# Performance work log

Measured on AMD Instinct MI355X. Metric: run time of the kernel, lower is better.

## Reference

```python
import jax, jax.numpy as jnp
import numpy as np

N_NODES = 40000
N_EDGES = 1_600_000
F_DIM = 64          # num_features per node; MLP input is 2*F_DIM = 128
HIDDEN = 64
BETA = 1.0          # temperature tmp passed to concrete_sample


def setup_inputs() -> dict:
    key = jax.random.key(0)
    k_e, k_n, k_w1, k_w2 = jax.random.split(key, 4)
    # unique edge list (matches torch COO->dense semantics exactly: no duplicate coords)
    rng = np.random.default_rng(0)
    keys = np.unique(rng.integers(0, N_NODES * N_NODES, size=int(N_EDGES * 1.1), dtype=np.int64))
    assert keys.size >= N_EDGES
    keys = keys[:N_EDGES]
    col = jnp.asarray((keys // N_NODES).astype(np.int32))
    row = jnp.asarray((keys % N_NODES).astype(np.int32))
    embed = jax.random.normal(k_e, (N_NODES, F_DIM), jnp.float32)
    # torch.rand noise for the concrete/gumbel-sigmoid sample (kept strictly inside (0,1))
    noise = jax.random.uniform(k_n, (N_EDGES,), jnp.float32, 1e-6, 1.0 - 1e-6)
    lim1 = 1.0 / np.sqrt(2 * F_DIM)
    W1 = jax.random.uniform(k_w1, (2 * F_DIM, HIDDEN), jnp.float32, -lim1, lim1)
    b1 = jnp.zeros((HIDDEN,), jnp.float32)
    lim2 = 1.0 / np.sqrt(HIDDEN)
    W2 = jax.random.uniform(k_w2, (HIDDEN, 1), jnp.float32, -lim2, lim2)
    b2 = jnp.zeros((1,), jnp.float32)
    return {"embed": embed, "W1": W1, "b1": b1, "W2": W2, "b2": b2,
            "noise": noise, "col": col, "row": row}


def reference(embed, W1, b1, W2, b2, noise, col, row):
    # --- gather + concat + 2-layer MLP (elayers) ---
    f12 = jnp.concatenate([embed[col], embed[row]], axis=-1)   # [E, 2F]
    h = jax.nn.relu(f12 @ W1 + b1)                              # [E, 64]
    log_alpha = (h @ W2 + b2).reshape(-1)                       # [E]
    # --- concrete_sample, training=True, sample_bias=0 ---
    gate = jnp.log(noise) - jnp.log1p(-noise)
    values = jax.nn.sigmoid((gate + log_alpha) / BETA)          # sparse_mask_values
    # --- symmetrization: sym = (M + M^T)/2 gathered back at (col,row) ---
    # Equivalent to torch's sparse->dense->transpose->gather, but done sparsely
    # via a reverse-edge lookup on sorted pair keys (edges are unique).
    n = embed.shape[0]
    keys = col * n + row                                        # int32-safe: n*n < 2^31
    order = jnp.argsort(keys)
    skeys = keys[order]
    svals = values[order]
    rkeys = row * n + col
    pos = jnp.clip(jnp.searchsorted(skeys, rkeys), 0, keys.shape[0] - 1)
    rev = jnp.where(skeys[pos] == rkeys, svals[pos], jnp.float32(0.0))
    edge_mask = (values + rev) * 0.5
    return edge_mask
```

## Files before the change

kernel.cpp:

```cpp
#include <hip/hip_runtime.h>
#include <hip/hip_bf16.h>


typedef __attribute__((ext_vector_type(2))) float f32x2;

#define EPAD 68

__global__ __launch_bounds__(256) void precompute_kernel(
        const float* __restrict__ embed,
        const float* __restrict__ W1,
        const float* __restrict__ b1,
        unsigned* __restrict__ Ptop,
        unsigned* __restrict__ Pbot,
        const int* __restrict__ col,
        int* __restrict__ rowptr,
        int n_nodes, int n_edges, int gemm_blocks) {
    int t = threadIdx.x;

    if ((int)blockIdx.x >= gemm_blocks) {
        int v = (blockIdx.x - gemm_blocks) * 256 + t;
        if (v <= n_nodes) {
            int lo = 0, hi = n_edges;
            while (lo < hi) {
                int mid = (lo + hi) >> 1;
                if (col[mid] < v) lo = mid + 1; else hi = mid;
            }
            rowptr[v] = lo;
        }
        return;
    }

    __shared__ float W1s[128 * 64];
    __shared__ float E[64 * EPAD];
    int base = blockIdx.x * 64;

#pragma unroll
    for (int i = 0; i < 8; ++i) {
        int idx = i * 256 + t;
        ((float4*)W1s)[idx] = ((const float4*)W1)[idx];
    }
#pragma unroll
    for (int i = 0; i < 4; ++i) {
        int fi = i * 256 + t;
        int n = fi >> 4;
        int k4 = (fi & 15) * 4;
        float4 v;
        if (base + n < n_nodes)
            v = ((const float4*)(embed + (size_t)(base + n) * 64))[fi & 15];
        else
            v = make_float4(0.f, 0.f, 0.f, 0.f);
        *((float4*)(E + n * EPAD + k4)) = v;
    }
    __syncthreads();

    int tj = t & 15, tn = t >> 4;
    int j4 = tj * 4, n4 = tn * 4;
    float4 b1v = *(const float4*)(b1 + j4);
    float4 at[4], ab[4];
#pragma unroll
    for (int i = 0; i < 4; ++i) {
        at[i] = b1v;
        ab[i] = make_float4(0.f, 0.f, 0.f, 0.f);
    }

#pragma unroll 2
    for (int k4 = 0; k4 < 64; k4 += 4) {
        float4 e[4], wt[4], wb[4];
#pragma unroll
        for (int i = 0; i < 4; ++i) {
            e[i]  = *(const float4*)(E + (n4 + i) * EPAD + k4);
            wt[i] = *(const float4*)(W1s + (k4 + i) * 64 + j4);
            wb[i] = *(const float4*)(W1s + (64 + k4 + i) * 64 + j4);
        }
#pragma unroll
        for (int n = 0; n < 4; ++n) {
#pragma unroll
            for (int kk = 0; kk < 4; ++kk) {
                float ev = (kk == 0) ? e[n].x : (kk == 1) ? e[n].y
                         : (kk == 2) ? e[n].z : e[n].w;
                at[n].x += ev * wt[kk].x;  at[n].y += ev * wt[kk].y;
                at[n].z += ev * wt[kk].z;  at[n].w += ev * wt[kk].w;
                ab[n].x += ev * wb[kk].x;  ab[n].y += ev * wb[kk].y;
                ab[n].z += ev * wb[kk].z;  ab[n].w += ev * wb[kk].w;
            }
        }
    }

#pragma unroll
    for (int i = 0; i < 4; ++i) {
        int node = base + n4 + i;
        if (node >= n_nodes) break;
        int wt8 = __builtin_amdgcn_cvt_pk_fp8_f32(at[i].x, at[i].y, 0, false);
        wt8     = __builtin_amdgcn_cvt_pk_fp8_f32(at[i].z, at[i].w, wt8, true);
        Ptop[(size_t)node * 16 + tj] = (unsigned)wt8;
        int wb8 = __builtin_amdgcn_cvt_pk_fp8_f32(ab[i].x, ab[i].y, 0, false);
        wb8     = __builtin_amdgcn_cvt_pk_fp8_f32(ab[i].z, ab[i].w, wb8, true);
        Pbot[(size_t)node * 16 + tj] = (unsigned)wb8;
    }
}

#define DOTW(au, bu, wp, acc0, acc1) do {                             \
    f32x2 alo = __builtin_amdgcn_cvt_pk_f32_fp8((au), false);         \
    f32x2 ahi = __builtin_amdgcn_cvt_pk_f32_fp8((au), true);          \
    f32x2 blo = __builtin_amdgcn_cvt_pk_f32_fp8((bu), false);         \
    f32x2 bhi = __builtin_amdgcn_cvt_pk_f32_fp8((bu), true);          \
    f32x2 s0 = alo + blo, s1 = ahi + bhi;                             \
    s0 = __builtin_elementwise_max(s0, (f32x2)0.f);                   \
    s1 = __builtin_elementwise_max(s1, (f32x2)0.f);                   \
    acc0 += s0 * ((const f32x2*)(wp))[0];                             \
    acc1 += s1 * ((const f32x2*)(wp))[1];                             \
} while (0)

__global__ void edge_value_kernel(const uint4* __restrict__ Ptop,
                                  const uint4* __restrict__ Pbot,
                                  const float* __restrict__ W2,
                                  const float* __restrict__ b2,
                                  const float* __restrict__ noise,
                                  const int* __restrict__ col,
                                  const int* __restrict__ row,
                                  unsigned short* __restrict__ row16,
                                  unsigned short* __restrict__ vals16,
                                  int n_edges) {
    int e = blockIdx.x * blockDim.x + threadIdx.x;
    if (e >= n_edges) return;
    int c = col[e], r = row[e];
    const uint4* pt = Ptop + (size_t)c * 4;
    const uint4* pb = Pbot + (size_t)r * 4;
    f32x2 acc0 = {b2[0], 0.f}, acc1 = {0.f, 0.f};
    f32x2 acc2 = {0.f, 0.f},  acc3 = {0.f, 0.f};
#pragma unroll
    for (int g = 0; g < 4; ++g) {
        uint4 a = pt[g];
        uint4 b = pb[g];
        const float* w = W2 + g * 16;
        DOTW(a.x, b.x, w,      acc0, acc1);
        DOTW(a.y, b.y, w + 4,  acc2, acc3);
        DOTW(a.z, b.z, w + 8,  acc0, acc1);
        DOTW(a.w, b.w, w + 12, acc2, acc3);
    }
    f32x2 acc = (acc0 + acc1) + (acc2 + acc3);
    float la = acc.x + acc.y;
    float u = noise[e];
    float v = u / (u + (1.f - u) * __expf(-la));
    unsigned q = (unsigned)(v * 65535.f + 0.5f);
    if (q > 65535u) q = 65535u;
    row16[e]  = (unsigned short)r;
    vals16[e] = (unsigned short)q;
}

__device__ __forceinline__ float rev_scan(const unsigned short* __restrict__ row16,
                                          const unsigned short* __restrict__ vals16,
                                          int c, int lo, int hi, int g, int rv) {
    if (rv < c) {
        while (++g < hi) { rv = row16[g]; if (rv >= c) break; }
        return (g < hi && rv == c) ? (float)vals16[g] : 0.f;
    } else {
        while (rv > c && g > lo) rv = row16[--g];
        return (rv == c) ? (float)vals16[g] : 0.f;
    }
}

__global__ __launch_bounds__(256) void symmetrize_kernel(
        const int* __restrict__ col,
        const unsigned short* __restrict__ row16,
        const unsigned short* __restrict__ vals16,
        const int* __restrict__ rowptr,
        float* __restrict__ out,
        int n_edges, float inv_n) {
    int t = threadIdx.x;
    int e0 = blockIdx.x * 1024 + t;
    int c[4], r[4], lo[4], hi[4], g[4], pr[4];
    float vq[4];
    bool p[4], s[4];

#pragma unroll
    for (int i = 0; i < 4; ++i) {
        int e = e0 + i * 256;
        p[i] = e < n_edges;
        c[i] = 0; r[i] = 0; vq[i] = 0.f;
        if (p[i]) {
            c[i]  = col[e];
            r[i]  = row16[e];
            vq[i] = (float)vals16[e];
        }
    }
#pragma unroll
    for (int i = 0; i < 4; ++i) {
        lo[i] = 0; hi[i] = 0;
        if (p[i]) { lo[i] = rowptr[r[i]]; hi[i] = rowptr[r[i] + 1]; }
    }
#pragma unroll
    for (int i = 0; i < 4; ++i) {
        s[i] = p[i] && hi[i] > lo[i];
        g[i] = 0; pr[i] = 0;
        if (s[i]) {
            g[i] = lo[i] + (int)((float)c[i] * (float)(hi[i] - lo[i]) * inv_n);
            if (g[i] >= hi[i]) g[i] = hi[i] - 1;
            pr[i] = row16[g[i]];
        }
    }
#pragma unroll
    for (int i = 0; i < 4; ++i) {
        if (!p[i]) continue;
        float rev = s[i] ? rev_scan(row16, vals16, c[i], lo[i], hi[i], g[i], pr[i]) : 0.f;
        out[e0 + i * 256] = (vq[i] + rev) * (0.5f / 65535.f);
    }
}

extern "C" void kernel_launch(void* const* d_in, const int* in_sizes, int n_in,
                              void* d_out, int out_size, void* d_ws, size_t ws_size,
                              hipStream_t stream) {
    const float* embed = (const float*)d_in[0];
    const float* W1    = (const float*)d_in[1];
    const float* b1    = (const float*)d_in[2];
    const float* W2    = (const float*)d_in[3];
    const float* b2    = (const float*)d_in[4];
    const float* noise = (const float*)d_in[5];
    const int*   col   = (const int*)d_in[6];
    const int*   row   = (const int*)d_in[7];

    int n_nodes = in_sizes[0] / 64;
    int n_edges = in_sizes[5];
    float* out = (float*)d_out;

    char* ws = (char*)d_ws;
    size_t p_sz   = (size_t)n_nodes * 16 * sizeof(unsigned);
    size_t e16_sz = (size_t)n_edges * sizeof(unsigned short);
    unsigned*       Ptop   = (unsigned*)ws;
    unsigned*       Pbot   = (unsigned*)(ws + p_sz);
    unsigned short* row16  = (unsigned short*)(ws + 2 * p_sz);
    unsigned short* vals16 = (unsigned short*)(ws + 2 * p_sz + e16_sz);
    int*            rowptr = (int*)(ws + 2 * p_sz + 2 * e16_sz);

    int gemm_blocks = (n_nodes + 63) / 64;
    int rp_blocks   = (n_nodes + 256) / 256;

    precompute_kernel<<<gemm_blocks + rp_blocks, 256, 0, stream>>>(
        embed, W1, b1, Ptop, Pbot, col, rowptr, n_nodes, n_edges, gemm_blocks);

    edge_value_kernel<<<(n_edges + 255) / 256, 256, 0, stream>>>(
        (const uint4*)Ptop, (const uint4*)Pbot, W2, b2, noise, col, row,
        row16, vals16, n_edges);

    symmetrize_kernel<<<(n_edges + 1023) / 1024, 256, 0, stream>>>(
        col, row16, vals16, rowptr, out, n_edges, 1.0f / (float)n_nodes);
}
```

Before: 71.75 us.

## Fuse edge MLP and symmetrization, recomputing reverse-edge value instead of storing

Merges the edge-value and symmetrize kernels into one launch. Each thread finds its reverse edge and recomputes that edge's MLP and sigmoid from the per-node fp8 projections and noise, rather than reading a quantized vals16 array. The row16 conversion moves into extra blocks of the precompute kernel. This removes one launch, the vals16 round-trip and the 16-bit value quantization, at the cost of doing the MLP a second time for reverse edges and adding random gathers of Ptop/Pbot and noise.

```diff
diff --git a/kernel.cpp b/kernel.cpp
--- a/kernel.cpp
+++ b/kernel.cpp
@@ -13,12 +13,32 @@
         unsigned* __restrict__ Ptop,
         unsigned* __restrict__ Pbot,
         const int* __restrict__ col,
+        const int* __restrict__ row,
         int* __restrict__ rowptr,
-        int n_nodes, int n_edges, int gemm_blocks) {
+        unsigned short* __restrict__ row16,
+        int n_nodes, int n_edges, int gemm_blocks, int rp_blocks) {
     int t = threadIdx.x;
-
-    if ((int)blockIdx.x >= gemm_blocks) {
-        int v = (blockIdx.x - gemm_blocks) * 256 + t;
+    int bid = blockIdx.x;
+
+    if (bid >= gemm_blocks + rp_blocks) {
+        int gt = (bid - gemm_blocks - rp_blocks) * 256 + t;
+        int e8 = gt * 8;
+        if (e8 + 7 < n_edges) {
+            int4 r0 = ((const int4*)(row + e8))[0];
+            int4 r1 = ((const int4*)(row + e8))[1];
+            uint4 packed;
+            packed.x = (unsigned)r0.x | ((unsigned)r0.y << 16);
+            packed.y = (unsigned)r0.z | ((unsigned)r0.w << 16);
+            packed.z = (unsigned)r1.x | ((unsigned)r1.y << 16);
+            packed.w = (unsigned)r1.z | ((unsigned)r1.w << 16);
+            *(uint4*)(row16 + e8) = packed;
+        } else {
+            for (int e = e8; e < n_edges; ++e) row16[e] = (unsigned short)row[e];
+        }
+        return;
+    }
+    if (bid >= gemm_blocks) {
+        int v = (bid - gemm_blocks) * 256 + t;
         if (v <= n_nodes) {
             int lo = 0, hi = n_edges;
             while (lo < hi) {
@@ -32,7 +52,7 @@
 
     __shared__ float W1s[128 * 64];
     __shared__ float E[64 * EPAD];
-    int base = blockIdx.x * 64;
+    int base = bid * 64;
 
 #pragma unroll
     for (int i = 0; i < 8; ++i) {
@@ -111,23 +131,12 @@
     acc1 += s1 * ((const f32x2*)(wp))[1];                             \
 } while (0)
 
-__global__ void edge_value_kernel(const uint4* __restrict__ Ptop,
-                                  const uint4* __restrict__ Pbot,
-                                  const float* __restrict__ W2,
-                                  const float* __restrict__ b2,
-                                  const float* __restrict__ noise,
-                                  const int* __restrict__ col,
-                                  const int* __restrict__ row,
-                                  unsigned short* __restrict__ row16,
-                                  unsigned short* __restrict__ vals16,
-                                  int n_edges) {
-    int e = blockIdx.x * blockDim.x + threadIdx.x;
-    if (e >= n_edges) return;
-    int c = col[e], r = row[e];
-    const uint4* pt = Ptop + (size_t)c * 4;
-    const uint4* pb = Pbot + (size_t)r * 4;
-    f32x2 acc0 = {b2[0], 0.f}, acc1 = {0.f, 0.f};
-    f32x2 acc2 = {0.f, 0.f},  acc3 = {0.f, 0.f};
+__device__ __forceinline__ float mlp_sigmoid(const uint4* __restrict__ pt,
+                                             const uint4* __restrict__ pb,
+                                             const float* __restrict__ W2,
+                                             float b2v, float u) {
+    f32x2 acc0 = {b2v, 0.f}, acc1 = {0.f, 0.f};
+    f32x2 acc2 = {0.f, 0.f}, acc3 = {0.f, 0.f};
 #pragma unroll
     for (int g = 0; g < 4; ++g) {
         uint4 a = pt[g];
@@ -140,71 +149,55 @@
     }
     f32x2 acc = (acc0 + acc1) + (acc2 + acc3);
     float la = acc.x + acc.y;
-    float u = noise[e];
-    float v = u / (u + (1.f - u) * __expf(-la));
-    unsigned q = (unsigned)(v * 65535.f + 0.5f);
-    if (q > 65535u) q = 65535u;
-    row16[e]  = (unsigned short)r;
-    vals16[e] = (unsigned short)q;
-}
-
-__device__ __forceinline__ float rev_scan(const unsigned short* __restrict__ row16,
-                                          const unsigned short* __restrict__ vals16,
-                                          int c, int lo, int hi, int g, int rv) {
-    if (rv < c) {
-        while (++g < hi) { rv = row16[g]; if (rv >= c) break; }
-        return (g < hi && rv == c) ? (float)vals16[g] : 0.f;
-    } else {
-        while (rv > c && g > lo) rv = row16[--g];
-        return (rv == c) ? (float)vals16[g] : 0.f;
-    }
-}
-
-__global__ __launch_bounds__(256) void symmetrize_kernel(
+    return u / (u + (1.f - u) * __expf(-la));
+}
+
+__global__ __launch_bounds__(256) void fused_edge_kernel(
+        const uint4* __restrict__ Ptop,
+        const uint4* __restrict__ Pbot,
+        const float* __restrict__ W2,
+        const float* __restrict__ b2,
+        const float* __restrict__ noise,
         const int* __restrict__ col,
+        const int* __restrict__ row,
         const unsigned short* __restrict__ row16,
-        const unsigned short* __restrict__ vals16,
         const int* __restrict__ rowptr,
         float* __restrict__ out,
         int n_edges, float inv_n) {
-    int t = threadIdx.x;
-    int e0 = blockIdx.x * 1024 + t;
-    int c[4], r[4], lo[4], hi[4], g[4], pr[4];
-    float vq[4];
-    bool p[4], s[4];
-
-#pragma unroll
-    for (int i = 0; i < 4; ++i) {
-        int e = e0 + i * 256;
-        p[i] = e < n_edges;
-        c[i] = 0; r[i] = 0; vq[i] = 0.f;
-        if (p[i]) {
-            c[i]  = col[e];
-            r[i]  = row16[e];
-            vq[i] = (float)vals16[e];
-        }
-    }
-#pragma unroll
-    for (int i = 0; i < 4; ++i) {
-        lo[i] = 0; hi[i] = 0;
-        if (p[i]) { lo[i] = rowptr[r[i]]; hi[i] = rowptr[r[i] + 1]; }
-    }
-#pragma unroll
-    for (int i = 0; i < 4; ++i) {
-        s[i] = p[i] && hi[i] > lo[i];
-        g[i] = 0; pr[i] = 0;
-        if (s[i]) {
-            g[i] = lo[i] + (int)((float)c[i] * (float)(hi[i] - lo[i]) * inv_n);
-            if (g[i] >= hi[i]) g[i] = hi[i] - 1;
-            pr[i] = row16[g[i]];
-        }
-    }
-#pragma unroll
-    for (int i = 0; i < 4; ++i) {
-        if (!p[i]) continue;
-        float rev = s[i] ? rev_scan(row16, vals16, c[i], lo[i], hi[i], g[i], pr[i]) : 0.f;
-        out[e0 + i * 256] = (vq[i] + rev) * (0.5f / 65535.f);
-    }
+    int e = blockIdx.x * blockDim.x + threadIdx.x;
+    if (e >= n_edges) return;
+    int c = col[e], r = row[e];
+    float u = noise[e];
+    float b2v = b2[0];
+
+    int lo = rowptr[r], hi = rowptr[r + 1];
+    bool seg = hi > lo;
+    int g = 0, pr = -1;
+    if (seg) {
+        g = lo + (int)((float)c * (float)(hi - lo) * inv_n);
+        if (g >= hi) g = hi - 1;
+        pr = row16[g];
+    }
+
+    float v = mlp_sigmoid(Ptop + (size_t)c * 4, Pbot + (size_t)r * 4, W2, b2v, u);
+
+    int ridx = -1;
+    if (seg) {
+        if (pr < c) {
+            while (++g < hi) { pr = row16[g]; if (pr >= c) break; }
+            if (g < hi && pr == c) ridx = g;
+        } else {
+            while (pr > c && g > lo) pr = row16[--g];
+            if (pr == c) ridx = g;
+        }
+    }
+
+    float rev = 0.f;
+    if (ridx >= 0) {
+        float u2 = noise[ridx];
+        rev = mlp_sigmoid(Ptop + (size_t)r * 4, Pbot + (size_t)c * 4, W2, b2v, u2);
+    }
+    out[e] = (v + rev) * 0.5f;
 }
 
 extern "C" void kernel_launch(void* const* d_in, const int* in_sizes, int n_in,
@@ -229,19 +222,17 @@
     unsigned*       Ptop   = (unsigned*)ws;
     unsigned*       Pbot   = (unsigned*)(ws + p_sz);
     unsigned short* row16  = (unsigned short*)(ws + 2 * p_sz);
-    unsigned short* vals16 = (unsigned short*)(ws + 2 * p_sz + e16_sz);
-    int*            rowptr = (int*)(ws + 2 * p_sz + 2 * e16_sz);
+    int*            rowptr = (int*)(ws + 2 * p_sz + e16_sz);
 
     int gemm_blocks = (n_nodes + 63) / 64;
     int rp_blocks   = (n_nodes + 256) / 256;
-
-    precompute_kernel<<<gemm_blocks + rp_blocks, 256, 0, stream>>>(
-        embed, W1, b1, Ptop, Pbot, col, rowptr, n_nodes, n_edges, gemm_blocks);
-
-    edge_value_kernel<<<(n_edges + 255) / 256, 256, 0, stream>>>(
+    int r16_blocks  = (n_edges + 2047) / 2048;
+
+    precompute_kernel<<<gemm_blocks + rp_blocks + r16_blocks, 256, 0, stream>>>(
+        embed, W1, b1, Ptop, Pbot, col, row, rowptr, row16,
+        n_nodes, n_edges, gemm_blocks, rp_blocks);
+
+    fused_edge_kernel<<<(n_edges + 255) / 256, 256, 0, stream>>>(
         (const uint4*)Ptop, (const uint4*)Pbot, W2, b2, noise, col, row,
-        row16, vals16, n_edges);
-
-    symmetrize_kernel<<<(n_edges + 1023) / 1024, 256, 0, stream>>>(
-        col, row16, vals16, rowptr, out, n_edges, 1.0f / (float)n_nodes);
-}
+        row16, rowptr, out, n_edges, 1.0f / (float)n_nodes);
+}
```

Result: slower. 82.65 us (+15.2%).

## Add hashed bitmap filter to skip reverse-edge search when absent

Applied to the files above, without the earlier changes.

Builds a 2^24-bit hash bitmap of edge keys in the edge-value kernel via atomicOr, zeroed by extra blocks in the precompute kernel. The symmetrize kernel probes the bitmap for the reverse key and only runs the rowptr lookup and interpolated scan on a hit. This avoids most dependent random reads, since random edges rarely have a reverse. It also drops the row16 copy and scans the original int32 row array instead. The cost is 1.6M global atomics, a 2MB bitmap clear, and wider scan reads.

```diff
diff --git a/kernel.cpp b/kernel.cpp
--- a/kernel.cpp
+++ b/kernel.cpp
@@ -5,6 +5,8 @@
 typedef __attribute__((ext_vector_type(2))) float f32x2;
 
 #define EPAD 68
+#define BM_WORDS (1u << 19)
+#define HASH_MUL 2654435761u
 
 __global__ __launch_bounds__(256) void precompute_kernel(
         const float* __restrict__ embed,
@@ -14,11 +16,19 @@
         unsigned* __restrict__ Pbot,
         const int* __restrict__ col,
         int* __restrict__ rowptr,
-        int n_nodes, int n_edges, int gemm_blocks) {
+        unsigned* __restrict__ bitmap,
+        int n_nodes, int n_edges, int gemm_blocks, int rp_blocks) {
     int t = threadIdx.x;
-
-    if ((int)blockIdx.x >= gemm_blocks) {
-        int v = (blockIdx.x - gemm_blocks) * 256 + t;
+    int bid = blockIdx.x;
+
+    if (bid >= gemm_blocks + rp_blocks) {
+        int idx = (bid - gemm_blocks - rp_blocks) * 256 + t;
+        if (idx < (int)(BM_WORDS / 4))
+            ((uint4*)bitmap)[idx] = make_uint4(0, 0, 0, 0);
+        return;
+    }
+    if (bid >= gemm_blocks) {
+        int v = (bid - gemm_blocks) * 256 + t;
         if (v <= n_nodes) {
             int lo = 0, hi = n_edges;
             while (lo < hi) {
@@ -32,7 +42,7 @@
 
     __shared__ float W1s[128 * 64];
     __shared__ float E[64 * EPAD];
-    int base = blockIdx.x * 64;
+    int base = bid * 64;
 
 #pragma unroll
     for (int i = 0; i < 8; ++i) {
@@ -118,9 +128,9 @@
                                   const float* __restrict__ noise,
                                   const int* __restrict__ col,
                                   const int* __restrict__ row,
-                                  unsigned short* __restrict__ row16,
                                   unsigned short* __restrict__ vals16,
-                                  int n_edges) {
+                                  unsigned* __restrict__ bitmap,
+                                  int n_edges, unsigned n_nodes) {
     int e = blockIdx.x * blockDim.x + threadIdx.x;
     if (e >= n_edges) return;
     int c = col[e], r = row[e];
@@ -144,34 +154,39 @@
     float v = u / (u + (1.f - u) * __expf(-la));
     unsigned q = (unsigned)(v * 65535.f + 0.5f);
     if (q > 65535u) q = 65535u;
-    row16[e]  = (unsigned short)r;
     vals16[e] = (unsigned short)q;
-}
-
-__device__ __forceinline__ float rev_scan(const unsigned short* __restrict__ row16,
-                                          const unsigned short* __restrict__ vals16,
-                                          int c, int lo, int hi, int g, int rv) {
+
+    unsigned k = (unsigned)c * n_nodes + (unsigned)r;
+    unsigned h = (k * HASH_MUL) >> 8;
+    atomicOr(&bitmap[h >> 5], 1u << (h & 31u));
+}
+
+__device__ __forceinline__ float rev_scan32(const int* __restrict__ row,
+                                            const unsigned short* __restrict__ vals16,
+                                            int c, int lo, int hi, int g, int rv) {
     if (rv < c) {
-        while (++g < hi) { rv = row16[g]; if (rv >= c) break; }
+        while (++g < hi) { rv = row[g]; if (rv >= c) break; }
         return (g < hi && rv == c) ? (float)vals16[g] : 0.f;
     } else {
-        while (rv > c && g > lo) rv = row16[--g];
+        while (rv > c && g > lo) rv = row[--g];
         return (rv == c) ? (float)vals16[g] : 0.f;
     }
 }
 
 __global__ __launch_bounds__(256) void symmetrize_kernel(
         const int* __restrict__ col,
-        const unsigned short* __restrict__ row16,
+        const int* __restrict__ row,
         const unsigned short* __restrict__ vals16,
         const int* __restrict__ rowptr,
+        const unsigned* __restrict__ bitmap,
         float* __restrict__ out,
-        int n_edges, float inv_n) {
+        int n_edges, unsigned n_nodes, float inv_n) {
     int t = threadIdx.x;
     int e0 = blockIdx.x * 1024 + t;
     int c[4], r[4], lo[4], hi[4], g[4], pr[4];
+    unsigned h[4], bw[4];
     float vq[4];
-    bool p[4], s[4];
+    bool p[4], hit[4], s[4];
 
 #pragma unroll
     for (int i = 0; i < 4; ++i) {
@@ -180,29 +195,39 @@
         c[i] = 0; r[i] = 0; vq[i] = 0.f;
         if (p[i]) {
             c[i]  = col[e];
-            r[i]  = row16[e];
+            r[i]  = row[e];
             vq[i] = (float)vals16[e];
         }
     }
 #pragma unroll
     for (int i = 0; i < 4; ++i) {
+        bw[i] = 0; h[i] = 0;
+        if (p[i]) {
+            unsigned kq = (unsigned)r[i] * n_nodes + (unsigned)c[i];
+            h[i] = (kq * HASH_MUL) >> 8;
+            bw[i] = bitmap[h[i] >> 5];
+        }
+    }
+#pragma unroll
+    for (int i = 0; i < 4; ++i) {
+        hit[i] = p[i] && ((bw[i] >> (h[i] & 31u)) & 1u);
         lo[i] = 0; hi[i] = 0;
-        if (p[i]) { lo[i] = rowptr[r[i]]; hi[i] = rowptr[r[i] + 1]; }
-    }
-#pragma unroll
-    for (int i = 0; i < 4; ++i) {
-        s[i] = p[i] && hi[i] > lo[i];
+        if (hit[i]) { lo[i] = rowptr[r[i]]; hi[i] = rowptr[r[i] + 1]; }
+    }
+#pragma unroll
+    for (int i = 0; i < 4; ++i) {
+        s[i] = hit[i] && hi[i] > lo[i];
         g[i] = 0; pr[i] = 0;
         if (s[i]) {
             g[i] = lo[i] + (int)((float)c[i] * (float)(hi[i] - lo[i]) * inv_n);
             if (g[i] >= hi[i]) g[i] = hi[i] - 1;
-            pr[i] = row16[g[i]];
+            pr[i] = row[g[i]];
         }
     }
 #pragma unroll
     for (int i = 0; i < 4; ++i) {
         if (!p[i]) continue;
-        float rev = s[i] ? rev_scan(row16, vals16, c[i], lo[i], hi[i], g[i], pr[i]) : 0.f;
+        float rev = s[i] ? rev_scan32(row, vals16, c[i], lo[i], hi[i], g[i], pr[i]) : 0.f;
         out[e0 + i * 256] = (vq[i] + rev) * (0.5f / 65535.f);
     }
 }
@@ -224,24 +249,28 @@
     float* out = (float*)d_out;
 
     char* ws = (char*)d_ws;
-    size_t p_sz   = (size_t)n_nodes * 16 * sizeof(unsigned);
-    size_t e16_sz = (size_t)n_edges * sizeof(unsigned short);
+    size_t p_sz  = (size_t)n_nodes * 16 * sizeof(unsigned);
+    size_t v_sz  = (size_t)n_edges * sizeof(unsigned short);
+    size_t bm_sz = (size_t)BM_WORDS * sizeof(unsigned);
     unsigned*       Ptop   = (unsigned*)ws;
     unsigned*       Pbot   = (unsigned*)(ws + p_sz);
-    unsigned short* row16  = (unsigned short*)(ws + 2 * p_sz);
-    unsigned short* vals16 = (unsigned short*)(ws + 2 * p_sz + e16_sz);
-    int*            rowptr = (int*)(ws + 2 * p_sz + 2 * e16_sz);
+    unsigned short* vals16 = (unsigned short*)(ws + 2 * p_sz);
+    unsigned*       bitmap = (unsigned*)(ws + 2 * p_sz + v_sz);
+    int*            rowptr = (int*)(ws + 2 * p_sz + v_sz + bm_sz);
 
     int gemm_blocks = (n_nodes + 63) / 64;
     int rp_blocks   = (n_nodes + 256) / 256;
-
-    precompute_kernel<<<gemm_blocks + rp_blocks, 256, 0, stream>>>(
-        embed, W1, b1, Ptop, Pbot, col, rowptr, n_nodes, n_edges, gemm_blocks);
+    int bz_blocks   = (int)(BM_WORDS / 4 + 255) / 256;
+
+    precompute_kernel<<<gemm_blocks + rp_blocks + bz_blocks, 256, 0, stream>>>(
+        embed, W1, b1, Ptop, Pbot, col, rowptr, bitmap,
+        n_nodes, n_edges, gemm_blocks, rp_blocks);
 
     edge_value_kernel<<<(n_edges + 255) / 256, 256, 0, stream>>>(
         (const uint4*)Ptop, (const uint4*)Pbot, W2, b2, noise, col, row,
-        row16, vals16, n_edges);
+        vals16, bitmap, n_edges, (unsigned)n_nodes);
 
     symmetrize_kernel<<<(n_edges + 1023) / 1024, 256, 0, stream>>>(
-        col, row16, vals16, rowptr, out, n_edges, 1.0f / (float)n_nodes);
-}
+        col, row, vals16, rowptr, bitmap, out, n_edges, (unsigned)n_nodes,
+        1.0f / (float)n_nodes);
+}
```

Measured after the change: 112.0 us. +56.1%, slower.
